# Kernel tuning notes

Hardware: AMD Instinct MI355X
Metric: run time of the kernel (lower is better)

The kernel has to match this reference:

```python
import jax, jax.numpy as jnp
import numpy as np

LEVELS = 16
FEATURES = 2
HASHMAP_SIZE = 524288
BASE_RES = 16
PER_LEVEL_SCALE = 1.3819

_P1, _P2, _P3 = np.uint32(73856093), np.uint32(19349663), np.uint32(83492791)
# 8 trilinear corner offsets, bit order (x, y, z)
_OFFSETS = np.array([[ox, oy, oz] for ox in (0, 1) for oy in (0, 1) for oz in (0, 1)], dtype=np.int32)


def setup_inputs() -> dict:
    key = jax.random.key(0)
    kx, kt = jax.random.split(key)
    x = jax.random.uniform(kx, (2000000, 3), dtype=jnp.float32)
    tables = jax.random.normal(kt, (LEVELS, HASHMAP_SIZE, FEATURES), dtype=jnp.float32) * 0.01
    return {"x": x, "tables": tables}


def _hash_coords(corners_u32):
    # corners_u32: [N, 8, 3] uint32; spatial hash with uint32 wraparound.
    h = (corners_u32[..., 0] * _P1) ^ (corners_u32[..., 1] * _P2) ^ (corners_u32[..., 2] * _P3)
    return (h % np.uint32(HASHMAP_SIZE)).astype(jnp.int32)  # [N, 8]


def _encode(x, tables):
    offsets_i = jnp.asarray(_OFFSETS)                 # [8, 3] int32
    offsets_f = offsets_i.astype(x.dtype)             # [8, 3]
    embeds = []
    for l in range(LEVELS):
        res = int(BASE_RES * PER_LEVEL_SCALE ** l)
        pos = x * res                                  # [N, 3]
        pos_floor = jnp.floor(pos)
        w = pos - pos_floor                            # [N, 3] trilinear weights
        base = pos_floor.astype(jnp.int32)             # non-negative (x in [0,1])
        corners = (base[:, None, :] + offsets_i).astype(jnp.uint32)  # [N, 8, 3]
        idx = _hash_coords(corners)                    # [N, 8]
        vals = tables[l][idx]                          # [N, 8, F] gather
        # weight per corner = prod over axes of (w if offset else 1-w)
        wgt = jnp.prod(offsets_f * w[:, None, :] + (1.0 - offsets_f) * (1.0 - w[:, None, :]), axis=-1)  # [N, 8]
        embeds.append(jnp.einsum('nc,ncf->nf', wgt, vals))  # [N, F]
    return jnp.concatenate(embeds, axis=-1)           # [N, LEVELS*F]


def reference(x, tables):
    return _encode(x, tables)
```

## Files before the change

### kernel.cpp

```cpp
#include <hip/hip_runtime.h>
#include <stdint.h>

#define LEVELS 16
#define FEAT 2
#define TABLE_SIZE 524288
#define TMASK (TABLE_SIZE - 1)

typedef float f32x2 __attribute__((ext_vector_type(2)));
typedef float f32x4 __attribute__((ext_vector_type(4)));
typedef float f32x4u __attribute__((ext_vector_type(4), aligned(8)));

__device__ __constant__ int kRes[LEVELS] = {
    16, 22, 30, 42, 58, 80, 111, 153, 212, 294, 406, 561, 775, 1072, 1481, 2047
};

#define P1 73856093u
#define P2 19349663u
#define P3 83492791u

#define D0 17
#define N0 4913
#define D1 23
#define N1 12167
#define D2 31
#define N2 29791
#define D3 43
#define N3 79507
#define D4 59
#define N4 205379
#define D5 81
#define N5 531441
#define NDENSE5 (N0 + N1 + N2 + N3 + N4)
#define NDENSE6 (NDENSE5 + N5)

constexpr int   cDD[6]   = { D0, D1, D2, D3, D4, D5 };
constexpr int   cDOff[6] = { 0, N0, N0+N1, N0+N1+N2, N0+N1+N2+N3, NDENSE5 };
constexpr float cDRes[6] = { 16.0f, 22.0f, 30.0f, 42.0f, 58.0f, 80.0f };
constexpr int   cDCum[7] = { 0, N0, N0+N1, N0+N1+N2, N0+N1+N2+N3, NDENSE5, NDENSE6 };

__global__ __launch_bounds__(256) void remap_kernel(
    const float* __restrict__ tables,
    f32x2* __restrict__ dense,
    int total)
{
    const int d = blockIdx.x * 256 + threadIdx.x;
    if (d >= total) return;
    int l = 0;
#pragma unroll
    for (int k = 1; k < 6; ++k)
        if (d >= cDCum[k]) l = k;
    const int D   = cDD[l];
    const int rel = d - cDCum[l];
    const uint32_t bx = rel / (D * D);
    const uint32_t r  = rel - bx * (D * D);
    const uint32_t by = r / D;
    const uint32_t bz = r - by * D;
    const uint32_t slot = ((bx * P1) ^ (by * P2) ^ (bz * P3)) & TMASK;
    const f32x2* __restrict__ tab = reinterpret_cast<const f32x2*>(tables) + (size_t)l * TABLE_SIZE;
    dense[d] = tab[slot];
}

__global__ __launch_bounds__(256) void encode_level_kernel(
    const float* __restrict__ x,
    const float* __restrict__ tables,
    f32x2* __restrict__ ws,
    int n, int nb, int l0)
{
    const int l   = l0 + blockIdx.x / nb;
    const int blk = blockIdx.x - (l - l0) * nb;
    const int t   = threadIdx.x;
    const int p0  = blk * 512;

    __shared__ float sx[512 * 3];
    const long long total3 = (long long)n * 3;
    const long long gbase  = (long long)p0 * 3;
#pragma unroll
    for (int k = 0; k < 6; ++k) {
        long long g = gbase + k * 256 + t;
        sx[k * 256 + t] = (g < total3) ? __builtin_nontemporal_load(x + g) : 0.0f;
    }
    __syncthreads();

    const float resf = (float)kRes[l];
    const f32x2* __restrict__ tab = reinterpret_cast<const f32x2*>(tables) + (size_t)l * TABLE_SIZE;

    uint32_t idx[2][8];
    float    wgt[2][8];
#pragma unroll
    for (int s = 0; s < 2; ++s) {
        const int tp = s * 256 + t;
        const float fx = sx[3 * tp + 0] * resf;
        const float fy = sx[3 * tp + 1] * resf;
        const float fz = sx[3 * tp + 2] * resf;
        const float flx = floorf(fx), fly = floorf(fy), flz = floorf(fz);
        const float wx = fx - flx, wy = fy - fly, wz = fz - flz;
        const float ux = 1.0f - wx, uy = 1.0f - wy, uz = 1.0f - wz;
        const uint32_t hx0 = (uint32_t)(int)flx * P1, hx1 = hx0 + P1;
        const uint32_t hy0 = (uint32_t)(int)fly * P2, hy1 = hy0 + P2;
        const uint32_t hz0 = (uint32_t)(int)flz * P3, hz1 = hz0 + P3;
#pragma unroll
        for (int c = 0; c < 8; ++c) {
            const uint32_t hx = (c & 4) ? hx1 : hx0;
            const uint32_t hy = (c & 2) ? hy1 : hy0;
            const uint32_t hz = (c & 1) ? hz1 : hz0;
            idx[s][c] = (hx ^ hy ^ hz) & TMASK;
            wgt[s][c] = ((c & 4) ? wx : ux) * ((c & 2) ? wy : uy) * ((c & 1) ? wz : uz);
        }
    }

    f32x2 v[2][8];
#pragma unroll
    for (int s = 0; s < 2; ++s)
#pragma unroll
        for (int c = 0; c < 8; ++c)
            v[s][c] = tab[idx[s][c]];

#pragma unroll
    for (int s = 0; s < 2; ++s) {
        float f0 = 0.0f, f1 = 0.0f;
#pragma unroll
        for (int c = 0; c < 8; ++c) {
            f0 = fmaf(wgt[s][c], v[s][c].x, f0);
            f1 = fmaf(wgt[s][c], v[s][c].y, f1);
        }
        const int i = p0 + s * 256 + t;
        if (i < n) {
            f32x2 r; r.x = f0; r.y = f1;
            __builtin_nontemporal_store(r, ws + (size_t)l * n + i);
        }
    }
}

template<int NDLEV>
__global__ __launch_bounds__(256) void finalize_kernel(
    const float* __restrict__ x,
    const f32x2* __restrict__ dense,
    const f32x2* __restrict__ ws,
    float* __restrict__ out,
    int n)
{
    __shared__ float s[256 * 33];
    __shared__ float sx[256 * 3];
    const int t  = threadIdx.x;
    const int p0 = blockIdx.x * 256;
    const int m  = min(256, n - p0);

    const long long total3 = (long long)n * 3;
    const long long gbase  = (long long)p0 * 3;
#pragma unroll
    for (int k = 0; k < 3; ++k) {
        long long g = gbase + k * 256 + t;
        sx[k * 256 + t] = (g < total3) ? __builtin_nontemporal_load(x + g) : 0.0f;
    }
    __syncthreads();

    if (t < m) {
        const int i = p0 + t;
        constexpr int NH = LEVELS - NDLEV;

        f32x2 h[NH];
#pragma unroll
        for (int j = 0; j < NH; ++j)
            h[j] = __builtin_nontemporal_load(ws + (size_t)(NDLEV + j) * n + i);

        const float px = sx[3 * t + 0];
        const float py = sx[3 * t + 1];
        const float pz = sx[3 * t + 2];

#pragma unroll
        for (int l = 0; l < NDLEV; ++l) {
            const int   D    = cDD[l];
            const int   DD   = D * D;
            const float resf = cDRes[l];
            const f32x2* __restrict__ tabd = dense + cDOff[l];
            const float fx = px * resf, fy = py * resf, fz = pz * resf;
            const float flx = floorf(fx), fly = floorf(fy), flz = floorf(fz);
            const float wx = fx - flx, wy = fy - fly, wz = fz - flz;
            const float ux = 1.0f - wx, uy = 1.0f - wy, uz = 1.0f - wz;
            const int base = ((int)flx * D + (int)fly) * D + (int)flz;

            f32x4u v[4];
#pragma unroll
            for (int p = 0; p < 4; ++p) {
                const int off = ((p & 2) ? DD : 0) + ((p & 1) ? D : 0);
                v[p] = *reinterpret_cast<const f32x4u*>(tabd + base + off);
            }
            float f0 = 0.0f, f1 = 0.0f;
#pragma unroll
            for (int p = 0; p < 4; ++p) {
                const float wxy = ((p & 2) ? wx : ux) * ((p & 1) ? wy : uy);
                f0 = fmaf(wxy, fmaf(uz, v[p].x, wz * v[p].z), f0);
                f1 = fmaf(wxy, fmaf(uz, v[p].y, wz * v[p].w), f1);
            }
            s[t * 33 + 2 * l + 0] = f0;
            s[t * 33 + 2 * l + 1] = f1;
        }
#pragma unroll
        for (int j = 0; j < NH; ++j) {
            s[t * 33 + 2 * (NDLEV + j) + 0] = h[j].x;
            s[t * 33 + 2 * (NDLEV + j) + 1] = h[j].y;
        }
    }
    __syncthreads();

    const int nchunk = m * 8;
    f32x4* __restrict__ o4 = reinterpret_cast<f32x4*>(out) + (size_t)p0 * 8;
#pragma unroll
    for (int j = 0; j < 8; ++j) {
        const int cl = j * 256 + t;
        if (cl < nchunk) {
            const int p = cl >> 3, ch = cl & 7;
            f32x4 q;
            q.x = s[p * 33 + ch * 4 + 0];
            q.y = s[p * 33 + ch * 4 + 1];
            q.z = s[p * 33 + ch * 4 + 2];
            q.w = s[p * 33 + ch * 4 + 3];
            __builtin_nontemporal_store(q, o4 + cl);
        }
    }
}

__global__ __launch_bounds__(256) void hashgrid_enc_kernel(
    const float* __restrict__ x,
    const float* __restrict__ tables,
    float* __restrict__ out,
    int n)
{
    __shared__ float sx[256 * 3];
    const int t = threadIdx.x;
    const int block0 = blockIdx.x * 256;
    const long long total3 = (long long)n * 3;
    const long long gbase = (long long)block0 * 3;
#pragma unroll
    for (int k = 0; k < 3; ++k) {
        long long g = gbase + k * 256 + t;
        sx[k * 256 + t] = (g < total3) ? x[g] : 0.0f;
    }
    __syncthreads();
    const int i = block0 + t;
    if (i >= n) return;
    const float px = sx[3 * t + 0];
    const float py = sx[3 * t + 1];
    const float pz = sx[3 * t + 2];
    float outv[2 * LEVELS];
#pragma unroll
    for (int l = 0; l < LEVELS; ++l) {
        const float resf = (float)kRes[l];
        const float fx = px * resf, fy = py * resf, fz = pz * resf;
        const float flx = floorf(fx), fly = floorf(fy), flz = floorf(fz);
        const float wx = fx - flx, wy = fy - fly, wz = fz - flz;
        const float ux = 1.0f - wx, uy = 1.0f - wy, uz = 1.0f - wz;
        const uint32_t hx0 = (uint32_t)(int)flx * P1, hx1 = hx0 + P1;
        const uint32_t hy0 = (uint32_t)(int)fly * P2, hy1 = hy0 + P2;
        const uint32_t hz0 = (uint32_t)(int)flz * P3, hz1 = hz0 + P3;
        const float* __restrict__ tab = tables + (size_t)l * (TABLE_SIZE * FEAT);
        float f0 = 0.0f, f1 = 0.0f;
#pragma unroll
        for (int c = 0; c < 8; ++c) {
            const uint32_t hx = (c & 4) ? hx1 : hx0;
            const uint32_t hy = (c & 2) ? hy1 : hy0;
            const uint32_t hz = (c & 1) ? hz1 : hz0;
            const uint32_t idx = (hx ^ hy ^ hz) & TMASK;
            const float2 v = *reinterpret_cast<const float2*>(tab + (size_t)idx * FEAT);
            const float w = ((c & 4) ? wx : ux) * ((c & 2) ? wy : uy) * ((c & 1) ? wz : uz);
            f0 = fmaf(w, v.x, f0);
            f1 = fmaf(w, v.y, f1);
        }
        outv[2 * l + 0] = f0;
        outv[2 * l + 1] = f1;
    }
    float4* __restrict__ o4 = reinterpret_cast<float4*>(out + (size_t)i * (2 * LEVELS));
#pragma unroll
    for (int k = 0; k < 8; ++k) {
        o4[k] = make_float4(outv[4 * k + 0], outv[4 * k + 1],
                            outv[4 * k + 2], outv[4 * k + 3]);
    }
}

extern "C" void kernel_launch(void* const* d_in, const int* in_sizes, int n_in,
                              void* d_out, int out_size, void* d_ws, size_t ws_size,
                              hipStream_t stream) {
    const float* x = (const float*)d_in[0];
    const float* tables = (const float*)d_in[1];
    float* out = (float*)d_out;
    const int n = in_sizes[0] / 3;

    const size_t ws_elems = (size_t)LEVELS * (size_t)n;
    const size_t needA = (ws_elems + NDENSE6 + 2) * sizeof(f32x2);
    const size_t needB = (ws_elems + NDENSE5 + 2) * sizeof(f32x2);

    if (ws_size >= needB) {
        const int planA = (ws_size >= needA);
        const int l0    = planA ? 6 : 5;
        const int total = planA ? NDENSE6 : NDENSE5;
        f32x2* ws    = (f32x2*)d_ws;
        f32x2* dense = ws + ws_elems;

        hipLaunchKernelGGL(remap_kernel, dim3((total + 255) / 256), dim3(256), 0, stream,
                           tables, dense, total);

        const int nb512 = (n + 511) / 512;
        hipLaunchKernelGGL(encode_level_kernel, dim3(nb512 * (LEVELS - l0)), dim3(256), 0, stream,
                           x, tables, ws, n, nb512, l0);

        const int nb256 = (n + 255) / 256;
        if (planA) {
            hipLaunchKernelGGL((finalize_kernel<6>), dim3(nb256), dim3(256), 0, stream,
                               x, dense, ws, out, n);
        } else {
            hipLaunchKernelGGL((finalize_kernel<5>), dim3(nb256), dim3(256), 0, stream,
                               x, dense, ws, out, n);
        }
    } else {
        const int nb = (n + 255) / 256;
        hipLaunchKernelGGL(hashgrid_enc_kernel, dim3(nb), dim3(256), 0, stream,
                           x, tables, out, n);
    }
}
```

Measured before the change: 1.020 ms.

## Pack dense coarse levels into fp16 corner tables and densify seven levels

Adds a second remap pass that turns each dense cell into a 16-byte record. The record holds the fp16 feature pairs for four of the cell's corners (z and y neighbours), so each dense level needs two uint4 loads instead of four 16-byte fp32 loads. The number of densified levels goes from 6 to 7, which cuts the hashed levels handled by the gather kernel to 9, and the staging buffer shrinks to match. The fp16 rounding of the table values adds numerical error. The extra remap pass and the larger precomputed table are redone on every call.

```diff
diff --git a/kernel.cpp b/kernel.cpp
--- a/kernel.cpp
+++ b/kernel.cpp
@@ -1,4 +1,5 @@
 #include <hip/hip_runtime.h>
+#include <hip/hip_fp16.h>
 #include <stdint.h>
 
 #define LEVELS 16
@@ -18,39 +19,27 @@
 #define P2 19349663u
 #define P3 83492791u
 
-#define D0 17
-#define N0 4913
-#define D1 23
-#define N1 12167
-#define D2 31
-#define N2 29791
-#define D3 43
-#define N3 79507
-#define D4 59
-#define N4 205379
-#define D5 81
-#define N5 531441
-#define NDENSE5 (N0 + N1 + N2 + N3 + N4)
-#define NDENSE6 (NDENSE5 + N5)
-
-constexpr int   cDD[6]   = { D0, D1, D2, D3, D4, D5 };
-constexpr int   cDOff[6] = { 0, N0, N0+N1, N0+N1+N2, N0+N1+N2+N3, NDENSE5 };
-constexpr float cDRes[6] = { 16.0f, 22.0f, 30.0f, 42.0f, 58.0f, 80.0f };
-constexpr int   cDCum[7] = { 0, N0, N0+N1, N0+N1+N2, N0+N1+N2+N3, NDENSE5, NDENSE6 };
-
-__global__ __launch_bounds__(256) void remap_kernel(
+#define NQLEV 7
+#define HASH0 7
+#define NHASH (LEVELS - HASH0)
+
+constexpr int   cQD[NQLEV]     = { 17, 23, 31, 43, 59, 81, 112 };
+constexpr float cQRes[NQLEV]   = { 16.0f, 22.0f, 30.0f, 42.0f, 58.0f, 80.0f, 111.0f };
+constexpr int   cQCum[NQLEV+1] = { 0, 4913, 17080, 46871, 126378, 331757, 863198, 2268126 };
+#define NCELLS 2268126
+
+__global__ __launch_bounds__(256) void remap1_kernel(
     const float* __restrict__ tables,
-    f32x2* __restrict__ dense,
-    int total)
+    f32x2* __restrict__ dense)
 {
     const int d = blockIdx.x * 256 + threadIdx.x;
-    if (d >= total) return;
+    if (d >= NCELLS) return;
     int l = 0;
 #pragma unroll
-    for (int k = 1; k < 6; ++k)
-        if (d >= cDCum[k]) l = k;
-    const int D   = cDD[l];
-    const int rel = d - cDCum[l];
+    for (int k = 1; k < NQLEV; ++k)
+        if (d >= cQCum[k]) l = k;
+    const int D   = cQD[l];
+    const int rel = d - cQCum[l];
     const uint32_t bx = rel / (D * D);
     const uint32_t r  = rel - bx * (D * D);
     const uint32_t by = r / D;
@@ -58,6 +47,31 @@
     const uint32_t slot = ((bx * P1) ^ (by * P2) ^ (bz * P3)) & TMASK;
     const f32x2* __restrict__ tab = reinterpret_cast<const f32x2*>(tables) + (size_t)l * TABLE_SIZE;
     dense[d] = tab[slot];
+}
+
+__global__ __launch_bounds__(256) void remap2_kernel(
+    const f32x2* __restrict__ dense,
+    uint4* __restrict__ qtab)
+{
+    const int d = blockIdx.x * 256 + threadIdx.x;
+    if (d >= NCELLS) return;
+    int l = 0;
+#pragma unroll
+    for (int k = 1; k < NQLEV; ++k)
+        if (d >= cQCum[k]) l = k;
+    const int D   = cQD[l];
+    const int rel = d - cQCum[l];
+
+    const f32x2* __restrict__ dl = dense + cQCum[l];
+    const f32x4u a = *reinterpret_cast<const f32x4u*>(dl + rel);
+    const f32x4u b = *reinterpret_cast<const f32x4u*>(dl + rel + D);
+
+    union { __half2 h; uint32_t u; } p0, p1, p2, p3;
+    p0.h = __float22half2_rn(make_float2(a.x, a.y));
+    p1.h = __float22half2_rn(make_float2(a.z, a.w));
+    p2.h = __float22half2_rn(make_float2(b.x, b.y));
+    p3.h = __float22half2_rn(make_float2(b.z, b.w));
+    qtab[d] = make_uint4(p0.u, p1.u, p2.u, p3.u);
 }
 
 __global__ __launch_bounds__(256) void encode_level_kernel(
@@ -126,15 +140,14 @@
         const int i = p0 + s * 256 + t;
         if (i < n) {
             f32x2 r; r.x = f0; r.y = f1;
-            __builtin_nontemporal_store(r, ws + (size_t)l * n + i);
-        }
-    }
-}
-
-template<int NDLEV>
+            __builtin_nontemporal_store(r, ws + (size_t)(l - l0) * n + i);
+        }
+    }
+}
+
 __global__ __launch_bounds__(256) void finalize_kernel(
     const float* __restrict__ x,
-    const f32x2* __restrict__ dense,
+    const uint4* __restrict__ qtab,
     const f32x2* __restrict__ ws,
     float* __restrict__ out,
     int n)
@@ -156,49 +169,57 @@
 
     if (t < m) {
         const int i = p0 + t;
-        constexpr int NH = LEVELS - NDLEV;
-
-        f32x2 h[NH];
-#pragma unroll
-        for (int j = 0; j < NH; ++j)
-            h[j] = __builtin_nontemporal_load(ws + (size_t)(NDLEV + j) * n + i);
+
+        f32x2 h[NHASH];
+#pragma unroll
+        for (int j = 0; j < NHASH; ++j)
+            h[j] = __builtin_nontemporal_load(ws + (size_t)j * n + i);
 
         const float px = sx[3 * t + 0];
         const float py = sx[3 * t + 1];
         const float pz = sx[3 * t + 2];
 
 #pragma unroll
-        for (int l = 0; l < NDLEV; ++l) {
-            const int   D    = cDD[l];
+        for (int l = 0; l < NQLEV; ++l) {
+            const int   D    = cQD[l];
             const int   DD   = D * D;
-            const float resf = cDRes[l];
-            const f32x2* __restrict__ tabd = dense + cDOff[l];
+            const float resf = cQRes[l];
+            const uint4* __restrict__ qt = qtab + cQCum[l];
+
             const float fx = px * resf, fy = py * resf, fz = pz * resf;
             const float flx = floorf(fx), fly = floorf(fy), flz = floorf(fz);
             const float wx = fx - flx, wy = fy - fly, wz = fz - flz;
             const float ux = 1.0f - wx, uy = 1.0f - wy, uz = 1.0f - wz;
-            const int base = ((int)flx * D + (int)fly) * D + (int)flz;
-
-            f32x4u v[4];
-#pragma unroll
-            for (int p = 0; p < 4; ++p) {
-                const int off = ((p & 2) ? DD : 0) + ((p & 1) ? D : 0);
-                v[p] = *reinterpret_cast<const f32x4u*>(tabd + base + off);
-            }
-            float f0 = 0.0f, f1 = 0.0f;
-#pragma unroll
-            for (int p = 0; p < 4; ++p) {
-                const float wxy = ((p & 2) ? wx : ux) * ((p & 1) ? wy : uy);
-                f0 = fmaf(wxy, fmaf(uz, v[p].x, wz * v[p].z), f0);
-                f1 = fmaf(wxy, fmaf(uz, v[p].y, wz * v[p].w), f1);
-            }
+            const int q0 = (((int)flx * D + (int)fly) * D + (int)flz);
+
+            const uint4 A = qt[q0];
+            const uint4 B = qt[q0 + DD];
+
+            union { uint32_t u; __half2 hh; } c;
+            float2 a00, a01, a10, a11, b00, b01, b10, b11;
+            c.u = A.x; a00 = __half22float2(c.hh);
+            c.u = A.y; a01 = __half22float2(c.hh);
+            c.u = A.z; a10 = __half22float2(c.hh);
+            c.u = A.w; a11 = __half22float2(c.hh);
+            c.u = B.x; b00 = __half22float2(c.hh);
+            c.u = B.y; b01 = __half22float2(c.hh);
+            c.u = B.z; b10 = __half22float2(c.hh);
+            c.u = B.w; b11 = __half22float2(c.hh);
+
+            const float ya0 = fmaf(uz, a00.x, wz * a01.x), ya1 = fmaf(uz, a10.x, wz * a11.x);
+            const float yb0 = fmaf(uz, b00.x, wz * b01.x), yb1 = fmaf(uz, b10.x, wz * b11.x);
+            const float f0  = fmaf(ux, fmaf(uy, ya0, wy * ya1), wx * fmaf(uy, yb0, wy * yb1));
+            const float za0 = fmaf(uz, a00.y, wz * a01.y), za1 = fmaf(uz, a10.y, wz * a11.y);
+            const float zb0 = fmaf(uz, b00.y, wz * b01.y), zb1 = fmaf(uz, b10.y, wz * b11.y);
+            const float f1  = fmaf(ux, fmaf(uy, za0, wy * za1), wx * fmaf(uy, zb0, wy * zb1));
+
             s[t * 33 + 2 * l + 0] = f0;
             s[t * 33 + 2 * l + 1] = f1;
         }
 #pragma unroll
-        for (int j = 0; j < NH; ++j) {
-            s[t * 33 + 2 * (NDLEV + j) + 0] = h[j].x;
-            s[t * 33 + 2 * (NDLEV + j) + 1] = h[j].y;
+        for (int j = 0; j < NHASH; ++j) {
+            s[t * 33 + 2 * (NQLEV + j) + 0] = h[j].x;
+            s[t * 33 + 2 * (NQLEV + j) + 1] = h[j].y;
         }
     }
     __syncthreads();
@@ -285,32 +306,27 @@
     float* out = (float*)d_out;
     const int n = in_sizes[0] / 3;
 
-    const size_t ws_elems = (size_t)LEVELS * (size_t)n;
-    const size_t needA = (ws_elems + NDENSE6 + 2) * sizeof(f32x2);
-    const size_t needB = (ws_elems + NDENSE5 + 2) * sizeof(f32x2);
-
-    if (ws_size >= needB) {
-        const int planA = (ws_size >= needA);
-        const int l0    = planA ? 6 : 5;
-        const int total = planA ? NDENSE6 : NDENSE5;
-        f32x2* ws    = (f32x2*)d_ws;
-        f32x2* dense = ws + ws_elems;
-
-        hipLaunchKernelGGL(remap_kernel, dim3((total + 255) / 256), dim3(256), 0, stream,
-                           tables, dense, total);
+    const size_t stag_b = (size_t)NHASH * (size_t)n * sizeof(f32x2);
+    const size_t qoff   = (stag_b + 15) & ~(size_t)15;
+    const size_t s1off  = qoff + (size_t)NCELLS * sizeof(uint4);
+    const size_t need   = s1off + ((size_t)NCELLS + 2 * 112) * sizeof(f32x2);
+
+    if (ws_size >= need) {
+        f32x2* staging = (f32x2*)d_ws;
+        uint4* qtab    = (uint4*)((char*)d_ws + qoff);
+        f32x2* stage1  = (f32x2*)((char*)d_ws + s1off);
+
+        const int nbcell = (NCELLS + 255) / 256;
+        hipLaunchKernelGGL(remap1_kernel, dim3(nbcell), dim3(256), 0, stream, tables, stage1);
+        hipLaunchKernelGGL(remap2_kernel, dim3(nbcell), dim3(256), 0, stream, stage1, qtab);
 
         const int nb512 = (n + 511) / 512;
-        hipLaunchKernelGGL(encode_level_kernel, dim3(nb512 * (LEVELS - l0)), dim3(256), 0, stream,
-                           x, tables, ws, n, nb512, l0);
+        hipLaunchKernelGGL(encode_level_kernel, dim3(nb512 * NHASH), dim3(256), 0, stream,
+                           x, tables, staging, n, nb512, HASH0);
 
         const int nb256 = (n + 255) / 256;
-        if (planA) {
-            hipLaunchKernelGGL((finalize_kernel<6>), dim3(nb256), dim3(256), 0, stream,
-                               x, dense, ws, out, n);
-        } else {
-            hipLaunchKernelGGL((finalize_kernel<5>), dim3(nb256), dim3(256), 0, stream,
-                               x, dense, ws, out, n);
-        }
+        hipLaunchKernelGGL(finalize_kernel, dim3(nb256), dim3(256), 0, stream,
+                           x, qtab, staging, out, n);
     } else {
         const int nb = (n + 255) / 256;
         hipLaunchKernelGGL(hashgrid_enc_kernel, dim3(nb), dim3(256), 0, stream,
```

New measurement: 978.3 us. -4.1%, faster.
